# Optimization experiments

Hardware: AMD Instinct MI355X
Metric: run time of the kernel (lower is better)

Reference implementation:

```python
import jax, jax.numpy as jnp
import numpy as np

N_NODES = 100000
N_EDGES = 1600000
DIMS = [64, 64, 64, 32]  # [n_feat] + hid


def setup_inputs() -> dict:
    key = jax.random.key(0)
    ks = jax.random.split(key, 2 + 2 * (len(DIMS) - 1))
    x = jax.random.normal(ks[0], (N_NODES, DIMS[0]), dtype=jnp.float32)
    edge_index = jax.random.randint(ks[1], (2, N_EDGES), 0, N_NODES, dtype=jnp.int64)
    inp = {"x": x, "edge_index": edge_index}
    for i in range(len(DIMS) - 1):
        fan_in, fan_out = DIMS[i], DIMS[i + 1]
        scale = 1.0 / np.sqrt(fan_in)
        inp[f"W{i+1}"] = jax.random.normal(ks[2 + 2 * i], (fan_in, fan_out), dtype=jnp.float32) * scale
        inp[f"b{i+1}"] = jax.random.normal(ks[3 + 2 * i], (fan_out,), dtype=jnp.float32) * scale
    return inp


def _gcn_conv(x, W, b, src, dst, dis):
    # h = X W ; out[i] = sum_{j->i} norm_ij * h[j] + dis[i]^2 * h[i] + b
    h = x @ W
    norm = dis[src] * dis[dst]                      # [E]
    agg = jax.ops.segment_sum(h[src] * norm[:, None], dst, num_segments=x.shape[0])
    agg = agg + h * (dis * dis)[:, None]            # self-loop contribution
    return agg + b


def reference(x, edge_index, W1, b1, W2, b2, W3, b3):
    src, dst = edge_index[0], edge_index[1]
    n = x.shape[0]
    # degree with self-loops (edge weight 1), symmetric normalization
    deg = jax.ops.segment_sum(jnp.ones(src.shape[0], x.dtype), dst, num_segments=n) + 1.0
    dis = jax.lax.rsqrt(deg)
    h = jax.nn.relu(_gcn_conv(x, W1, b1, src, dst, dis))   # dropout is identity in eval
    h = jax.nn.relu(_gcn_conv(h, W2, b2, src, dst, dis))
    return _gcn_conv(h, W3, b3, src, dst, dis)
```

## Files before the change

### kernel.cpp

```cpp
#include <hip/hip_runtime.h>


typedef __attribute__((ext_vector_type(8))) _Float16 half8;

static inline int cdiv(int a, int b) { return (a + b - 1) / b; }

#define ACHUNK 8192
#define MAXNBK 512

__global__ void k_bucket_hist(const int* __restrict__ dst, int* __restrict__ counts_t,
                              int NBK, int NBA, int E) {
    __shared__ int cnt[MAXNBK];
    int t = threadIdx.x, b = blockIdx.x;
    for (int i = t; i < NBK; i += 256) cnt[i] = 0;
    __syncthreads();
    int e0 = b * ACHUNK;
#pragma unroll 8
    for (int j = 0; j < ACHUNK / 256; ++j) {
        int e = e0 + j * 256 + t;
        if (e < E) atomicAdd(&cnt[dst[e] >> 8], 1);
    }
    __syncthreads();
    for (int i = t; i < NBK; i += 256) counts_t[i * NBA + b] = cnt[i];
}

#define SCAN_T 256
#define SCAN_V 4
#define SCAN_CHUNK 1024

__global__ void k_scan_partial(const int* __restrict__ a, int* __restrict__ bsum, int n) {
    __shared__ int red[SCAN_T];
    int t = threadIdx.x, b = blockIdx.x;
    int base = b * SCAN_CHUNK + t * SCAN_V;
    int s = 0;
#pragma unroll
    for (int j = 0; j < SCAN_V; ++j) { int i = base + j; if (i < n) s += a[i]; }
    red[t] = s;
    __syncthreads();
    for (int off = SCAN_T / 2; off > 0; off >>= 1) {
        if (t < off) red[t] += red[t + off];
        __syncthreads();
    }
    if (t == 0) bsum[b] = red[0];
}

__global__ void k_scan_final(const int* __restrict__ a, const int* __restrict__ bsum,
                             int* __restrict__ out, int nb, int n) {
    __shared__ int sb[256];
    __shared__ int sh[SCAN_T];
    int t = threadIdx.x, bk = blockIdx.x;
    sb[t] = (t < nb) ? bsum[t] : 0;
    __syncthreads();
    for (int off = 1; off < 256; off <<= 1) {
        int u = (t >= off) ? sb[t - off] : 0;
        __syncthreads();
        sb[t] += u;
        __syncthreads();
    }
    int bbase = (bk == 0) ? 0 : sb[bk - 1];
    int base = bk * SCAN_CHUNK + t * SCAN_V;
    int v[SCAN_V];
    int s = 0;
#pragma unroll
    for (int j = 0; j < SCAN_V; ++j) {
        int i = base + j;
        v[j] = (i < n) ? a[i] : 0;
        s += v[j];
    }
    sh[t] = s;
    __syncthreads();
    for (int off = 1; off < SCAN_T; off <<= 1) {
        int u = (t >= off) ? sh[t - off] : 0;
        __syncthreads();
        sh[t] += u;
        __syncthreads();
    }
    int run = sh[t] - s + bbase;
#pragma unroll
    for (int j = 0; j < SCAN_V; ++j) {
        int i = base + j;
        if (i < n) { out[i] = run; run += v[j]; }
    }
}

__global__ void k_bucket_scatter(const int* __restrict__ src, const int* __restrict__ dst,
                                 const int* __restrict__ offsets, unsigned* __restrict__ bucketed,
                                 int NBK, int NBA, int E) {
    __shared__ int curs[MAXNBK];
    int t = threadIdx.x, b = blockIdx.x;
    for (int i = t; i < NBK; i += 256) curs[i] = offsets[i * NBA + b];
    __syncthreads();
    int e0 = b * ACHUNK;
#pragma unroll 8
    for (int j = 0; j < ACHUNK / 256; ++j) {
        int e = e0 + j * 256 + t;
        if (e < E) {
            int d = dst[e];
            int pos = atomicAdd(&curs[d >> 8], 1);
            bucketed[pos] = (unsigned)src[e] | ((unsigned)(d & 255) << 24);
        }
    }
}

__global__ void k_bucket_build(const unsigned* __restrict__ bucketed,
                               const int* __restrict__ offsets,
                               int* __restrict__ csr_src, int* __restrict__ row_start,
                               float* __restrict__ dis, int NBK, int NBA, int N, int E) {
    __shared__ int cnt[256];
    __shared__ int sc[256];
    int t = threadIdx.x, k = blockIdx.x;
    int base = offsets[k * NBA];
    int end = (k + 1 < NBK) ? offsets[(k + 1) * NBA] : E;
    cnt[t] = 0;
    __syncthreads();
    for (int i = base + t; i < end; i += 256)
        atomicAdd(&cnt[bucketed[i] >> 24], 1);
    __syncthreads();
    int c = cnt[t];
    sc[t] = c;
    __syncthreads();
    for (int off = 1; off < 256; off <<= 1) {
        int u = (t >= off) ? sc[t - off] : 0;
        __syncthreads();
        sc[t] += u;
        __syncthreads();
    }
    int excl = sc[t] - c;
    int node = k * 256 + t;
    if (node < N) {
        row_start[node] = base + excl;
        dis[node] = rsqrtf(1.0f + (float)c);
    }
    if (k == 0 && t == 0) row_start[N] = E;
    cnt[t] = base + excl;
    __syncthreads();
    for (int i = base + t; i < end; i += 256) {
        unsigned w = bucketed[i];
        int pos = atomicAdd(&cnt[w >> 24], 1);
        csr_src[pos] = (int)(w & 0xFFFFFFu);
    }
}

template <int K, int M>
__global__ void k_gemm_f(const float* __restrict__ X, const float* __restrict__ W,
                         const float* __restrict__ dis, _Float16* __restrict__ H, int n) {
    constexpr int TPR = M / 8;
    constexpr int ROWS = 256 / TPR;
    constexpr int KP = K + 1;
    __shared__ float Ws[K * M];
    __shared__ float Xs[ROWS * KP];
    int tid = threadIdx.x;
    for (int idx = tid; idx < K * M / 4; idx += 256)
        ((float4*)Ws)[idx] = ((const float4*)W)[idx];
    int row0 = blockIdx.x * ROWS;
    for (int idx = tid; idx < ROWS * (K / 4); idx += 256) {
        int r = idx / (K / 4), kq = idx % (K / 4);
        int row = row0 + r;
        float4 vv = (row < n) ? ((const float4*)X)[(size_t)row * (K / 4) + kq]
                              : make_float4(0.f, 0.f, 0.f, 0.f);
        Xs[r * KP + kq * 4 + 0] = vv.x;
        Xs[r * KP + kq * 4 + 1] = vv.y;
        Xs[r * KP + kq * 4 + 2] = vv.z;
        Xs[r * KP + kq * 4 + 3] = vv.w;
    }
    __syncthreads();
    int r = tid / TPR, c0 = (tid % TPR) * 8;
    int row = row0 + r;
    if (row >= n) return;
    float4 a0 = make_float4(0.f, 0.f, 0.f, 0.f);
    float4 a1 = make_float4(0.f, 0.f, 0.f, 0.f);
#pragma unroll
    for (int k = 0; k < K; ++k) {
        float xv = Xs[r * KP + k];
        float4 w0 = ((const float4*)Ws)[(k * M + c0) / 4];
        float4 w1 = ((const float4*)Ws)[(k * M + c0) / 4 + 1];
        a0.x = fmaf(xv, w0.x, a0.x);
        a0.y = fmaf(xv, w0.y, a0.y);
        a0.z = fmaf(xv, w0.z, a0.z);
        a0.w = fmaf(xv, w0.w, a0.w);
        a1.x = fmaf(xv, w1.x, a1.x);
        a1.y = fmaf(xv, w1.y, a1.y);
        a1.z = fmaf(xv, w1.z, a1.z);
        a1.w = fmaf(xv, w1.w, a1.w);
    }
    float dn = dis[row];
    half8 hv;
    hv[0] = (_Float16)(a0.x * dn);
    hv[1] = (_Float16)(a0.y * dn);
    hv[2] = (_Float16)(a0.z * dn);
    hv[3] = (_Float16)(a0.w * dn);
    hv[4] = (_Float16)(a1.x * dn);
    hv[5] = (_Float16)(a1.y * dn);
    hv[6] = (_Float16)(a1.z * dn);
    hv[7] = (_Float16)(a1.w * dn);
    ((half8*)H)[(size_t)row * (M / 8) + c0 / 8] = hv;
}

template <int MOUT>
__global__ void k_fused_agg_gemm(const _Float16* __restrict__ h, const float* __restrict__ dis,
                                 const int* __restrict__ row_start, const int* __restrict__ csr_src,
                                 const float* __restrict__ bagg, const float* __restrict__ W,
                                 _Float16* __restrict__ H, int n) {
    constexpr int K = 64, KP = K + 1;
    __shared__ float Ws[K * MOUT];
    __shared__ float Xs[32 * KP];
    int tid = threadIdx.x;
    for (int idx = tid; idx < K * MOUT / 4; idx += 256)
        ((float4*)Ws)[idx] = ((const float4*)W)[idx];

    int wave = tid >> 6, lane = tid & 63;
    int sub = lane >> 3, fl = lane & 7;
    int node0 = blockIdx.x * 32;
    int node = node0 + wave * 8 + sub;
    if (node < n) {
        const half8* h8 = (const half8*)h;
        float acc[8];
#pragma unroll
        for (int j = 0; j < 8; ++j) acc[j] = 0.f;
        int e = row_start[node], e1 = row_start[node + 1];
        for (; e + 3 < e1; e += 4) {
            int s0 = csr_src[e], s1 = csr_src[e + 1];
            int s2 = csr_src[e + 2], s3 = csr_src[e + 3];
            half8 v0 = h8[(size_t)s0 * 8 + fl];
            half8 v1 = h8[(size_t)s1 * 8 + fl];
            half8 v2 = h8[(size_t)s2 * 8 + fl];
            half8 v3 = h8[(size_t)s3 * 8 + fl];
#pragma unroll
            for (int j = 0; j < 8; ++j)
                acc[j] += ((float)v0[j] + (float)v1[j]) + ((float)v2[j] + (float)v3[j]);
        }
        for (; e < e1; ++e) {
            int s0 = csr_src[e];
            half8 v0 = h8[(size_t)s0 * 8 + fl];
#pragma unroll
            for (int j = 0; j < 8; ++j) acc[j] += (float)v0[j];
        }
        float dn = dis[node];
        half8 hv = h8[(size_t)node * 8 + fl];
        float4 b0 = ((const float4*)bagg)[fl * 2];
        float4 b1 = ((const float4*)bagg)[fl * 2 + 1];
        int rrow = wave * 8 + sub;
        float* xp = &Xs[rrow * KP + fl * 8];
        xp[0] = fmaxf((acc[0] + (float)hv[0]) * dn + b0.x, 0.f);
        xp[1] = fmaxf((acc[1] + (float)hv[1]) * dn + b0.y, 0.f);
        xp[2] = fmaxf((acc[2] + (float)hv[2]) * dn + b0.z, 0.f);
        xp[3] = fmaxf((acc[3] + (float)hv[3]) * dn + b0.w, 0.f);
        xp[4] = fmaxf((acc[4] + (float)hv[4]) * dn + b1.x, 0.f);
        xp[5] = fmaxf((acc[5] + (float)hv[5]) * dn + b1.y, 0.f);
        xp[6] = fmaxf((acc[6] + (float)hv[6]) * dn + b1.z, 0.f);
        xp[7] = fmaxf((acc[7] + (float)hv[7]) * dn + b1.w, 0.f);
    }
    __syncthreads();

    constexpr int TPR = MOUT / 8;
    int r = tid / TPR, c0 = (tid % TPR) * 8;
    int row = node0 + r;
    if (r >= 32 || row >= n) return;
    float4 a0 = make_float4(0.f, 0.f, 0.f, 0.f);
    float4 a1 = make_float4(0.f, 0.f, 0.f, 0.f);
#pragma unroll
    for (int k = 0; k < K; ++k) {
        float xv = Xs[r * KP + k];
        float4 w0 = ((const float4*)Ws)[(k * MOUT + c0) / 4];
        float4 w1 = ((const float4*)Ws)[(k * MOUT + c0) / 4 + 1];
        a0.x = fmaf(xv, w0.x, a0.x);
        a0.y = fmaf(xv, w0.y, a0.y);
        a0.z = fmaf(xv, w0.z, a0.z);
        a0.w = fmaf(xv, w0.w, a0.w);
        a1.x = fmaf(xv, w1.x, a1.x);
        a1.y = fmaf(xv, w1.y, a1.y);
        a1.z = fmaf(xv, w1.z, a1.z);
        a1.w = fmaf(xv, w1.w, a1.w);
    }
    float dn = dis[row];
    half8 hv;
    hv[0] = (_Float16)(a0.x * dn);
    hv[1] = (_Float16)(a0.y * dn);
    hv[2] = (_Float16)(a0.z * dn);
    hv[3] = (_Float16)(a0.w * dn);
    hv[4] = (_Float16)(a1.x * dn);
    hv[5] = (_Float16)(a1.y * dn);
    hv[6] = (_Float16)(a1.z * dn);
    hv[7] = (_Float16)(a1.w * dn);
    ((half8*)H)[(size_t)row * (MOUT / 8) + c0 / 8] = hv;
}

__global__ void k_aggregate32(const _Float16* __restrict__ h, const float* __restrict__ dis,
                              const int* __restrict__ row_start, const int* __restrict__ csr_src,
                              const float* __restrict__ b, float* __restrict__ out, int n) {
    constexpr int LPN = 4, NPW = 16;
    int gtid = blockIdx.x * blockDim.x + threadIdx.x;
    int wave = gtid >> 6;
    int lane = threadIdx.x & 63;
    int sub = lane / LPN, fl = lane % LPN;
    int node = wave * NPW + sub;
    if (node >= n) return;
    const half8* h8 = (const half8*)h;
    float acc[8];
#pragma unroll
    for (int j = 0; j < 8; ++j) acc[j] = 0.f;
    int e = row_start[node], e1 = row_start[node + 1];
    for (; e + 3 < e1; e += 4) {
        int s0 = csr_src[e], s1 = csr_src[e + 1];
        int s2 = csr_src[e + 2], s3 = csr_src[e + 3];
        half8 v0 = h8[(size_t)s0 * LPN + fl];
        half8 v1 = h8[(size_t)s1 * LPN + fl];
        half8 v2 = h8[(size_t)s2 * LPN + fl];
        half8 v3 = h8[(size_t)s3 * LPN + fl];
#pragma unroll
        for (int j = 0; j < 8; ++j)
            acc[j] += ((float)v0[j] + (float)v1[j]) + ((float)v2[j] + (float)v3[j]);
    }
    for (; e < e1; ++e) {
        int s0 = csr_src[e];
        half8 v0 = h8[(size_t)s0 * LPN + fl];
#pragma unroll
        for (int j = 0; j < 8; ++j) acc[j] += (float)v0[j];
    }
    float dn = dis[node];
    half8 hv = h8[(size_t)node * LPN + fl];
    float4 b0 = ((const float4*)b)[fl * 2];
    float4 b1 = ((const float4*)b)[fl * 2 + 1];
    float4* op = (float4*)(out + ((size_t)node * LPN + fl) * 8);
    op[0] = make_float4((acc[0] + (float)hv[0]) * dn + b0.x,
                        (acc[1] + (float)hv[1]) * dn + b0.y,
                        (acc[2] + (float)hv[2]) * dn + b0.z,
                        (acc[3] + (float)hv[3]) * dn + b0.w);
    op[1] = make_float4((acc[4] + (float)hv[4]) * dn + b1.x,
                        (acc[5] + (float)hv[5]) * dn + b1.y,
                        (acc[6] + (float)hv[6]) * dn + b1.z,
                        (acc[7] + (float)hv[7]) * dn + b1.w);
}

extern "C" void kernel_launch(void* const* d_in, const int* in_sizes, int n_in,
                              void* d_out, int out_size, void* d_ws, size_t ws_size,
                              hipStream_t stream) {
    const float* x   = (const float*)d_in[0];
    const int*   ei  = (const int*)d_in[1];
    const float* W1  = (const float*)d_in[2];
    const float* b1  = (const float*)d_in[3];
    const float* W2  = (const float*)d_in[4];
    const float* b2  = (const float*)d_in[5];
    const float* W3  = (const float*)d_in[6];
    const float* b3  = (const float*)d_in[7];
    float* out = (float*)d_out;

    const int N = in_sizes[0] / 64;
    const int E = in_sizes[1] / 2;
    const int* src = ei;
    const int* dst = ei + E;

    const int NBK = cdiv(N, 256);
    const int NBA = cdiv(E, ACHUNK);
    const int nmat = NBK * NBA;

    const size_t Np = (size_t)((N + 63) / 64) * 64;
    char* p = (char*)d_ws;
    int*      counts_t = (int*)p;      p += (size_t)nmat * sizeof(int);
    int*      offsets  = (int*)p;      p += (size_t)nmat * sizeof(int);
    int*      bsum     = (int*)p;      p += 1024 * sizeof(int);
    int*      row_start= (int*)p;      p += (Np + 64) * sizeof(int);
    float*    dis      = (float*)p;    p += Np * sizeof(float);
    unsigned* bucketed = (unsigned*)p; p += (size_t)E * sizeof(unsigned);
    int*      csr_src  = (int*)p;      p += (size_t)E * sizeof(int);
    _Float16* bufA     = (_Float16*)p; p += Np * 64 * sizeof(_Float16);
    _Float16* bufB     = (_Float16*)p; p += Np * 64 * sizeof(_Float16);
    (void)ws_size;

    const int B = 256;
    const int nb = cdiv(nmat, SCAN_CHUNK);

    k_bucket_hist<<<NBA, B, 0, stream>>>(dst, counts_t, NBK, NBA, E);
    k_scan_partial<<<nb, B, 0, stream>>>(counts_t, bsum, nmat);
    k_scan_final<<<nb, B, 0, stream>>>(counts_t, bsum, offsets, nb, nmat);
    k_bucket_scatter<<<NBA, B, 0, stream>>>(src, dst, offsets, bucketed, NBK, NBA, E);
    k_bucket_build<<<NBK, B, 0, stream>>>(bucketed, offsets, csr_src, row_start, dis,
                                          NBK, NBA, N, E);

    k_gemm_f<64, 64><<<cdiv(N, 32), B, 0, stream>>>(x, W1, dis, bufA, N);
    k_fused_agg_gemm<64><<<cdiv(N, 32), B, 0, stream>>>(
        bufA, dis, row_start, csr_src, b1, W2, bufB, N);
    k_fused_agg_gemm<32><<<cdiv(N, 32), B, 0, stream>>>(
        bufB, dis, row_start, csr_src, b2, W3, bufA, N);
    k_aggregate32<<<cdiv(cdiv(N, 16) * 64, B), B, 0, stream>>>(
        bufA, dis, row_start, csr_src, b3, out, N);
}
```

Before: 299.3 us.

## Use per-wave histograms in CSR build and fp16 weights in fused GEMM

The bucket histogram, scatter and build kernels now keep one shared-memory counter array per wave instead of one per block. Each wave handles a smaller 2048-edge chunk, which cuts LDS atomic contention and exposes more parallelism, at the price of a larger counts matrix to scan (the scan chunk is widened to match). The fused aggregate+GEMM kernel stores W in shared memory as fp16 with launch bounds set for higher occupancy, shrinking its LDS footprint. The fp16 weights add a small rounding error.

New measurement: 316.8 us. 5.8% more time.

```diff
diff --git a/kernel.cpp b/kernel.cpp
--- a/kernel.cpp
+++ b/kernel.cpp
@@ -2,31 +2,42 @@
 
 
 typedef __attribute__((ext_vector_type(8))) _Float16 half8;
+typedef __attribute__((ext_vector_type(4))) _Float16 half4;
 
 static inline int cdiv(int a, int b) { return (a + b - 1) / b; }
 
-#define ACHUNK 8192
+#define CHW 2048
 #define MAXNBK 512
 
 __global__ void k_bucket_hist(const int* __restrict__ dst, int* __restrict__ counts_t,
-                              int NBK, int NBA, int E) {
-    __shared__ int cnt[MAXNBK];
+                              int NBK, int NW, int E) {
+    __shared__ int cnt[4][MAXNBK];
     int t = threadIdx.x, b = blockIdx.x;
-    for (int i = t; i < NBK; i += 256) cnt[i] = 0;
-    __syncthreads();
-    int e0 = b * ACHUNK;
+    int w = t >> 6, lane = t & 63;
+    for (int i = t; i < 4 * MAXNBK; i += 256) ((int*)cnt)[i] = 0;
+    __syncthreads();
+    int c = b * 4 + w;
+    if (c < NW) {
+        int e0 = c * CHW;
 #pragma unroll 8
-    for (int j = 0; j < ACHUNK / 256; ++j) {
-        int e = e0 + j * 256 + t;
-        if (e < E) atomicAdd(&cnt[dst[e] >> 8], 1);
-    }
-    __syncthreads();
-    for (int i = t; i < NBK; i += 256) counts_t[i * NBA + b] = cnt[i];
+        for (int j = 0; j < CHW / 64; ++j) {
+            int e = e0 + j * 64 + lane;
+            if (e < E) atomicAdd(&cnt[w][dst[e] >> 8], 1);
+        }
+    }
+    __syncthreads();
+    for (int i = t; i < NBK; i += 256) {
+#pragma unroll
+        for (int ww = 0; ww < 4; ++ww) {
+            int cc = b * 4 + ww;
+            if (cc < NW) counts_t[i * NW + cc] = cnt[ww][i];
+        }
+    }
 }
 
 #define SCAN_T 256
-#define SCAN_V 4
-#define SCAN_CHUNK 1024
+#define SCAN_V 8
+#define SCAN_CHUNK 2048
 
 __global__ void k_scan_partial(const int* __restrict__ a, int* __restrict__ bsum, int n) {
     __shared__ int red[SCAN_T];
@@ -85,18 +96,27 @@
 
 __global__ void k_bucket_scatter(const int* __restrict__ src, const int* __restrict__ dst,
                                  const int* __restrict__ offsets, unsigned* __restrict__ bucketed,
-                                 int NBK, int NBA, int E) {
-    __shared__ int curs[MAXNBK];
+                                 int NBK, int NW, int E) {
+    __shared__ int curs[4][MAXNBK];
     int t = threadIdx.x, b = blockIdx.x;
-    for (int i = t; i < NBK; i += 256) curs[i] = offsets[i * NBA + b];
-    __syncthreads();
-    int e0 = b * ACHUNK;
+    int w = t >> 6, lane = t & 63;
+    for (int i = t; i < NBK; i += 256) {
+#pragma unroll
+        for (int ww = 0; ww < 4; ++ww) {
+            int cc = b * 4 + ww;
+            if (cc < NW) curs[ww][i] = offsets[i * NW + cc];
+        }
+    }
+    __syncthreads();
+    int c = b * 4 + w;
+    if (c >= NW) return;
+    int e0 = c * CHW;
 #pragma unroll 8
-    for (int j = 0; j < ACHUNK / 256; ++j) {
-        int e = e0 + j * 256 + t;
+    for (int j = 0; j < CHW / 64; ++j) {
+        int e = e0 + j * 64 + lane;
         if (e < E) {
             int d = dst[e];
-            int pos = atomicAdd(&curs[d >> 8], 1);
+            int pos = atomicAdd(&curs[w][d >> 8], 1);
             bucketed[pos] = (unsigned)src[e] | ((unsigned)(d & 255) << 24);
         }
     }
@@ -105,18 +125,21 @@
 __global__ void k_bucket_build(const unsigned* __restrict__ bucketed,
                                const int* __restrict__ offsets,
                                int* __restrict__ csr_src, int* __restrict__ row_start,
-                               float* __restrict__ dis, int NBK, int NBA, int N, int E) {
-    __shared__ int cnt[256];
+                               float* __restrict__ dis, int NBK, int NW, int N, int E) {
+    __shared__ int cnt4[4][256];
     __shared__ int sc[256];
     int t = threadIdx.x, k = blockIdx.x;
-    int base = offsets[k * NBA];
-    int end = (k + 1 < NBK) ? offsets[(k + 1) * NBA] : E;
-    cnt[t] = 0;
-    __syncthreads();
-    for (int i = base + t; i < end; i += 256)
-        atomicAdd(&cnt[bucketed[i] >> 24], 1);
-    __syncthreads();
-    int c = cnt[t];
+    int w = t >> 6, lane = t & 63;
+    int base = offsets[k * NW];
+    int end = (k + 1 < NBK) ? offsets[(k + 1) * NW] : E;
+#pragma unroll
+    for (int ww = 0; ww < 4; ++ww) cnt4[ww][t] = 0;
+    __syncthreads();
+    for (int i = base + w * 64 + lane; i < end; i += 256)
+        atomicAdd(&cnt4[w][bucketed[i] >> 24], 1);
+    __syncthreads();
+    int c0 = cnt4[0][t], c1 = cnt4[1][t], c2 = cnt4[2][t], c3 = cnt4[3][t];
+    int c = c0 + c1 + c2 + c3;
     sc[t] = c;
     __syncthreads();
     for (int off = 1; off < 256; off <<= 1) {
@@ -132,12 +155,16 @@
         dis[node] = rsqrtf(1.0f + (float)c);
     }
     if (k == 0 && t == 0) row_start[N] = E;
-    cnt[t] = base + excl;
-    __syncthreads();
-    for (int i = base + t; i < end; i += 256) {
-        unsigned w = bucketed[i];
-        int pos = atomicAdd(&cnt[w >> 24], 1);
-        csr_src[pos] = (int)(w & 0xFFFFFFu);
+    int b0 = base + excl;
+    cnt4[0][t] = b0;
+    cnt4[1][t] = b0 + c0;
+    cnt4[2][t] = b0 + c0 + c1;
+    cnt4[3][t] = b0 + c0 + c1 + c2;
+    __syncthreads();
+    for (int i = base + w * 64 + lane; i < end; i += 256) {
+        unsigned v = bucketed[i];
+        int pos = atomicAdd(&cnt4[w][v >> 24], 1);
+        csr_src[pos] = (int)(v & 0xFFFFFFu);
     }
 }
 
@@ -197,16 +224,24 @@
 }
 
 template <int MOUT>
-__global__ void k_fused_agg_gemm(const _Float16* __restrict__ h, const float* __restrict__ dis,
-                                 const int* __restrict__ row_start, const int* __restrict__ csr_src,
-                                 const float* __restrict__ bagg, const float* __restrict__ W,
-                                 _Float16* __restrict__ H, int n) {
+__global__ __launch_bounds__(256, 8)
+void k_fused_agg_gemm(const _Float16* __restrict__ h, const float* __restrict__ dis,
+                      const int* __restrict__ row_start, const int* __restrict__ csr_src,
+                      const float* __restrict__ bagg, const float* __restrict__ W,
+                      _Float16* __restrict__ H, int n) {
     constexpr int K = 64, KP = K + 1;
-    __shared__ float Ws[K * MOUT];
+    __shared__ _Float16 Ws[K * MOUT];
     __shared__ float Xs[32 * KP];
     int tid = threadIdx.x;
-    for (int idx = tid; idx < K * MOUT / 4; idx += 256)
-        ((float4*)Ws)[idx] = ((const float4*)W)[idx];
+    for (int idx = tid; idx < K * MOUT / 4; idx += 256) {
+        float4 v = ((const float4*)W)[idx];
+        half4 hh;
+        hh[0] = (_Float16)v.x;
+        hh[1] = (_Float16)v.y;
+        hh[2] = (_Float16)v.z;
+        hh[3] = (_Float16)v.w;
+        ((half4*)Ws)[idx] = hh;
+    }
 
     int wave = tid >> 6, lane = tid & 63;
     int sub = lane >> 3, fl = lane & 7;
@@ -256,32 +291,20 @@
     int r = tid / TPR, c0 = (tid % TPR) * 8;
     int row = node0 + r;
     if (r >= 32 || row >= n) return;
-    float4 a0 = make_float4(0.f, 0.f, 0.f, 0.f);
-    float4 a1 = make_float4(0.f, 0.f, 0.f, 0.f);
+    float a[8];
+#pragma unroll
+    for (int j = 0; j < 8; ++j) a[j] = 0.f;
 #pragma unroll
     for (int k = 0; k < K; ++k) {
         float xv = Xs[r * KP + k];
-        float4 w0 = ((const float4*)Ws)[(k * MOUT + c0) / 4];
-        float4 w1 = ((const float4*)Ws)[(k * MOUT + c0) / 4 + 1];
-        a0.x = fmaf(xv, w0.x, a0.x);
-        a0.y = fmaf(xv, w0.y, a0.y);
-        a0.z = fmaf(xv, w0.z, a0.z);
-        a0.w = fmaf(xv, w0.w, a0.w);
-        a1.x = fmaf(xv, w1.x, a1.x);
-        a1.y = fmaf(xv, w1.y, a1.y);
-        a1.z = fmaf(xv, w1.z, a1.z);
-        a1.w = fmaf(xv, w1.w, a1.w);
+        half8 wv = ((const half8*)Ws)[k * (MOUT / 8) + c0 / 8];
+#pragma unroll
+        for (int j = 0; j < 8; ++j) a[j] = fmaf(xv, (float)wv[j], a[j]);
     }
     float dn = dis[row];
     half8 hv;
-    hv[0] = (_Float16)(a0.x * dn);
-    hv[1] = (_Float16)(a0.y * dn);
-    hv[2] = (_Float16)(a0.z * dn);
-    hv[3] = (_Float16)(a0.w * dn);
-    hv[4] = (_Float16)(a1.x * dn);
-    hv[5] = (_Float16)(a1.y * dn);
-    hv[6] = (_Float16)(a1.z * dn);
-    hv[7] = (_Float16)(a1.w * dn);
+#pragma unroll
+    for (int j = 0; j < 8; ++j) hv[j] = (_Float16)(a[j] * dn);
     ((half8*)H)[(size_t)row * (MOUT / 8) + c0 / 8] = hv;
 }
 
@@ -351,8 +374,9 @@
     const int* dst = ei + E;
 
     const int NBK = cdiv(N, 256);
-    const int NBA = cdiv(E, ACHUNK);
-    const int nmat = NBK * NBA;
+    const int NW  = cdiv(E, CHW);
+    const int NBA = cdiv(NW, 4);
+    const int nmat = NBK * NW;
 
     const size_t Np = (size_t)((N + 63) / 64) * 64;
     char* p = (char*)d_ws;
@@ -370,12 +394,12 @@
     const int B = 256;
     const int nb = cdiv(nmat, SCAN_CHUNK);
 
-    k_bucket_hist<<<NBA, B, 0, stream>>>(dst, counts_t, NBK, NBA, E);
+    k_bucket_hist<<<NBA, B, 0, stream>>>(dst, counts_t, NBK, NW, E);
     k_scan_partial<<<nb, B, 0, stream>>>(counts_t, bsum, nmat);
     k_scan_final<<<nb, B, 0, stream>>>(counts_t, bsum, offsets, nb, nmat);
-    k_bucket_scatter<<<NBA, B, 0, stream>>>(src, dst, offsets, bucketed, NBK, NBA, E);
+    k_bucket_scatter<<<NBA, B, 0, stream>>>(src, dst, offsets, bucketed, NBK, NW, E);
     k_bucket_build<<<NBK, B, 0, stream>>>(bucketed, offsets, csr_src, row_start, dis,
-                                          NBK, NBA, N, E);
+                                          NBK, NW, N, E);
 
     k_gemm_f<64, 64><<<cdiv(N, 32), B, 0, stream>>>(x, W1, dis, bufA, N);
     k_fused_agg_gemm<64><<<cdiv(N, 32), B, 0, stream>>>(
```
